# Kernel optimization log

Measured on AMD Instinct MI355X. Metric: run time of the kernel, lower is better.

The kernel has to match this reference:

```python
import jax, jax.numpy as jnp
import numpy as np

N, E = 50000, 800000
F_IN, C1, H1 = 128, 16, 4        # conv1: 128 -> 16 per head, 4 heads (concat -> 64)
F_MID = C1 * H1                   # 64
N_CLASSES, H2 = 10, 1             # conv2: 64 -> 10, 1 head, no concat
NEG_SLOPE = 0.2


def setup_inputs() -> dict:
    key = jax.random.key(0)
    ks = jax.random.split(key, 12)
    s1 = 1.0 / np.sqrt(F_IN)
    s2 = 1.0 / np.sqrt(F_MID)
    return {
        "x": jax.random.normal(ks[0], (N, F_IN), dtype=jnp.float32),
        "edge_index": jax.random.randint(ks[1], (2, E), 0, N, dtype=jnp.int64),
        # conv1 params (GATv2: separate lin_l / lin_r, per-head attention vector, bias)
        "W1l": jax.random.normal(ks[2], (F_IN, H1 * C1), dtype=jnp.float32) * s1,
        "W1r": jax.random.normal(ks[3], (F_IN, H1 * C1), dtype=jnp.float32) * s1,
        "att1": jax.random.normal(ks[4], (H1, C1), dtype=jnp.float32) * s1,
        "b1": jnp.zeros((H1 * C1,), dtype=jnp.float32),
        # conv2 params
        "W2l": jax.random.normal(ks[5], (F_MID, H2 * N_CLASSES), dtype=jnp.float32) * s2,
        "W2r": jax.random.normal(ks[6], (F_MID, H2 * N_CLASSES), dtype=jnp.float32) * s2,
        "att2": jax.random.normal(ks[7], (H2, N_CLASSES), dtype=jnp.float32) * s2,
        "b2": jnp.zeros((N_CLASSES,), dtype=jnp.float32),
    }


def gatv2_conv(x, Wl, Wr, att, b, src, dst, concat):
    """GATv2Conv (add_self_loops=False, eval mode). src -> dst message passing."""
    H, C = att.shape
    n = x.shape[0]
    xl = (x @ Wl).reshape(n, H, C)   # source-side transform (also the value)
    xr = (x @ Wr).reshape(n, H, C)   # target-side transform
    # per-edge GATv2 score: att . LeakyReLU(xl[src] + xr[dst])
    e = jax.nn.leaky_relu(xl[src] + xr[dst], NEG_SLOPE)          # [E, H, C]
    logits = jnp.einsum("ehc,hc->eh", e, att)                    # [E, H]
    # segment softmax over incoming edges of each dst node
    m = jax.ops.segment_max(logits, dst, num_segments=n)         # [N, H]
    ex = jnp.exp(logits - m[dst])
    denom = jax.ops.segment_sum(ex, dst, num_segments=n)         # [N, H]
    alpha = ex / denom[dst]                                      # [E, H]
    out = jax.ops.segment_sum(alpha[:, :, None] * xl[src], dst, num_segments=n)  # [N, H, C]
    out = out.reshape(n, H * C) if concat else out.mean(axis=1)
    return out + b


def reference(x, edge_index, W1l, W1r, att1, b1, W2l, W2r, att2, b2):
    src, dst = edge_index[0], edge_index[1]
    h = jax.nn.elu(gatv2_conv(x, W1l, W1r, att1, b1, src, dst, concat=True))
    return gatv2_conv(h, W2l, W2r, att2, b2, src, dst, concat=False)
```

## Files before the change

kernel.cpp:

```cpp
#include <hip/hip_runtime.h>
#include <math.h>

#define NN 50000
#define NE 800000
#define FIN 128
#define NC 10
#define NEG 0.2f
#define LOG2E 1.4426950408889634f

#define NB 196
#define CHUNK 4096
#define P1B ((NE + CHUNK - 1) / CHUNK)
#define CAP 5120
#define GMT ((NN + 63) / 64)
#define LBW 200
#define WPAD 136

typedef unsigned int uint;
typedef _Float16 h2 __attribute__((ext_vector_type(2)));
typedef _Float16 h8 __attribute__((ext_vector_type(8)));
typedef float f32x4 __attribute__((ext_vector_type(4)));
typedef __fp16 hb2 __attribute__((ext_vector_type(2)));
union U2H { uint u; h2 h; };
union U4H8 { uint4 u; h8 h; };

__device__ __forceinline__ uint pkrtz_u(float a, float b) {
    union { hb2 f; uint u; } r;
    r.f = __builtin_amdgcn_cvt_pkrtz(a, b);
    return r.u;
}

__device__ __forceinline__ float dot2f(h2 a, h2 b, float c) {
#if __has_builtin(__builtin_amdgcn_fdot2)
    return __builtin_amdgcn_fdot2(a, b, c, false);
#else
    return fmaf((float)a.x, (float)b.x, fmaf((float)a.y, (float)b.y, c));
#endif
}

__device__ __forceinline__ float fexp2(float x) {
#if __has_builtin(__builtin_amdgcn_exp2f)
    return __builtin_amdgcn_exp2f(x);
#else
    return exp2f(x);
#endif
}

__device__ __forceinline__ uint ld_off(const uint* __restrict__ base, uint byteoff) {
    return *(const uint*)((const char*)base + (size_t)byteoff);
}

__device__ __forceinline__ h2 lrelu2(h2 v) {
    return __builtin_elementwise_max(v, v * (_Float16)0.2f);
}

template<int CTRL>
__device__ __forceinline__ float dpp_add(float x) {
    int y = __builtin_amdgcn_update_dpp(0, __float_as_int(x), CTRL, 0xF, 0xF, true);
    return x + __int_as_float(y);
}
__device__ __forceinline__ float red8(float t) {
    t = dpp_add<0xB1>(t);
    t = dpp_add<0x4E>(t);
    t = dpp_add<0x141>(t);
    return t;
}

__device__ __forceinline__ int excl_scan256(int v, int* sc) {
    const int t = threadIdx.x;
    sc[t] = v;
    __syncthreads();
    for (int o = 1; o < 256; o <<= 1) {
        int u = (t >= o) ? sc[t - o] : 0;
        __syncthreads();
        sc[t] += u;
        __syncthreads();
    }
    return sc[t] - v;
}


__device__ void pass1_body(const int* __restrict__ ei, uint* __restrict__ temp,
                           int* __restrict__ lbmat, char* smraw) {
    uint* pk = (uint*)smraw;
    int* h   = (int*)(smraw + 16384);
    int* h2_ = (int*)(smraw + 17408);
    int* sc  = (int*)(smraw + 18432);
    const int t = threadIdx.x;
    const int B = blockIdx.x;
    const int e0 = B * CHUNK;
    const int cnt = min(CHUNK, NE - e0);

    h[t] = 0; h2_[t] = 0;
    __syncthreads();
    for (int i = t; i < cnt; i += 256) {
        int d = ei[NE + e0 + i];
        atomicAdd(&h[d >> 8], 1);
    }
    __syncthreads();
    const int hv = h[t];
    const int ex = excl_scan256(hv, sc);
    if (t < NB) lbmat[B * LBW + t] = ex;
    if (t == NB - 1) lbmat[B * LBW + NB] = ex + hv;
    h2_[t] = ex;
    __syncthreads();
    for (int i = t; i < cnt; i += 256) {
        int s = ei[e0 + i];
        int d = ei[NE + e0 + i];
        int b = d >> 8;
        int pos = atomicAdd(&h2_[b], 1);
        pk[pos] = ((uint)s << 8) | ((uint)d & 255u);
    }
    __syncthreads();
    for (int i = t; i < cnt; i += 256) temp[B * CHUNK + i] = pk[i];
}

__device__ void gemm1_body(const float* __restrict__ x,
                           const float* __restrict__ W1l,
                           const float* __restrict__ W1r,
                           _Float16* __restrict__ xlh,
                           _Float16* __restrict__ xrh,
                           int n0, char* smraw) {
    _Float16 (*WtL)[WPAD] = (_Float16(*)[WPAD])smraw;
    _Float16 (*WtR)[WPAD] = (_Float16(*)[WPAD])(smraw + 64 * WPAD * 2);
    const int t = threadIdx.x;

    for (int i = t; i < FIN * 64; i += 256) {
        int k = i >> 6, c = i & 63;
        WtL[c][k] = (_Float16)W1l[i];
        WtR[c][k] = (_Float16)W1r[i];
    }
    __syncthreads();

    const int lane = t & 63;
    const int n0w = n0 + (t >> 6) * 16;
    const int arow = n0w + (lane & 15);
    const int kgrp = (lane >> 4) * 8;
    const int col16 = lane & 15;

    f32x4 acc[8] = {};
    for (int kk = 0; kk < FIN; kk += 32) {
        U4H8 a;
        if (arow < NN) {
            const float4* xp = (const float4*)(x + (size_t)arow * FIN + kk + kgrp);
            float4 v0 = xp[0], v1 = xp[1];
            a.u = make_uint4(pkrtz_u(v0.x, v0.y), pkrtz_u(v0.z, v0.w),
                             pkrtz_u(v1.x, v1.y), pkrtz_u(v1.z, v1.w));
        } else {
            a.u = make_uint4(0u, 0u, 0u, 0u);
        }
        const int kof = kk + kgrp;
#pragma unroll
        for (int ct = 0; ct < 4; ++ct) {
            U4H8 b; b.u = *(const uint4*)&WtL[ct * 16 + col16][kof];
            acc[ct] = __builtin_amdgcn_mfma_f32_16x16x32_f16(a.h, b.h, acc[ct], 0, 0, 0);
        }
#pragma unroll
        for (int ct = 0; ct < 4; ++ct) {
            U4H8 b; b.u = *(const uint4*)&WtR[ct * 16 + col16][kof];
            acc[4 + ct] = __builtin_amdgcn_mfma_f32_16x16x32_f16(a.h, b.h, acc[4 + ct], 0, 0, 0);
        }
    }
    const int crow0 = n0w + (lane >> 4) * 4;
#pragma unroll
    for (int ct = 0; ct < 8; ++ct) {
        _Float16* __restrict__ op = (ct < 4) ? xlh : xrh;
        const int col = (ct & 3) * 16 + col16;
#pragma unroll
        for (int r = 0; r < 4; ++r) {
            int node = crow0 + r;
            if (node < NN) op[(size_t)node * 64 + col] = (_Float16)acc[ct][r];
        }
    }
}

__global__ __launch_bounds__(256) void k_fusedA(const float* __restrict__ x,
                                                const int* __restrict__ ei,
                                                const float* __restrict__ W1l,
                                                const float* __restrict__ W1r,
                                                _Float16* __restrict__ xlh,
                                                _Float16* __restrict__ xrh,
                                                uint* __restrict__ temp,
                                                int* __restrict__ lbmat) {
    __shared__ __align__(16) char smraw[64 * WPAD * 2 * 2];
    if (blockIdx.x < P1B) {
        pass1_body(ei, temp, lbmat, smraw);
    } else {
        int g = blockIdx.x - P1B;
        gemm1_body(x, W1l, W1r, xlh, xrh, g * 64, smraw);
    }
}


__global__ __launch_bounds__(256) void k_pass2(const uint* __restrict__ temp,
                                               const int* __restrict__ lbmat,
                                               int* __restrict__ rowptr,
                                               int* __restrict__ deg,
                                               int* __restrict__ csr_src) {
    __shared__ uint P[CAP];
    __shared__ int nh[256], nbx[256], ncur[256], sc[256];
    const int t = threadIdx.x;
    const int b = blockIdx.x;

    int lbv = 0, len = 0;
    if (t < P1B) {
        lbv = lbmat[t * LBW + b];
        len = lbmat[t * LBW + b + 1] - lbv;
    }
    const int colstart = excl_scan256(len, sc);
    __syncthreads();
    const int cnt = sc[255];
    __syncthreads();
    (void)excl_scan256(lbv, sc);
    __syncthreads();
    const int csrbase = sc[255];
    __syncthreads();
    nh[t] = 0; ncur[t] = 0;
    __syncthreads();
    if (t < P1B) {
        const uint* src = temp + t * CHUNK + lbv;
        for (int i = 0; i < len; ++i) P[colstart + i] = src[i];
    }
    __syncthreads();
    for (int i = t; i < cnt; i += 256) atomicAdd(&nh[P[i] & 255u], 1);
    __syncthreads();
    const int c = nh[t];
    const int nb_ex = excl_scan256(c, sc);
    nbx[t] = nb_ex;
    const int gnode = b * 256 + t;
    if (gnode < NN) { rowptr[gnode] = csrbase + nb_ex; deg[gnode] = c; }
    __syncthreads();
    for (int i = t; i < cnt; i += 256) {
        uint v = P[i];
        int l = (int)(v & 255u);
        int r = atomicAdd(&ncur[l], 1);
        csr_src[csrbase + nbx[l] + r] = (int)(v >> 8);
    }
}


__global__ __launch_bounds__(256) void k_agg1(const uint* __restrict__ xlh2,
                                              const uint* __restrict__ xrh2,
                                              const int* __restrict__ rowptr,
                                              const int* __restrict__ deg,
                                              const int* __restrict__ csr_src,
                                              const float* __restrict__ att1,
                                              const float* __restrict__ b1,
                                              uint* __restrict__ hbh2) {
    const int node = blockIdx.x * 4 + (threadIdx.x >> 6);
    if (node >= NN) return;
    const int lane = threadIdx.x & 63;
    const int fl = lane & 31;
    const uint fl4 = (uint)fl * 4u;
    const int hid = lane >> 5;
    float2 av = *(const float2*)&att1[2 * fl];
    U2H att; att.u = pkrtz_u(av.x * LOG2E, av.y * LOG2E);
    U2H xrf; xrf.u = xrh2[(size_t)node * 32 + fl];
    const int start = rowptr[node];
    const int dg = deg[node];
    const int permbase = (lane & 32) >> 3;

    float denom = 0.f, acc0 = 0.f, acc1 = 0.f;
    for (int base = 0; base < dg; base += 64) {
        int idx = base + lane;
        uint srcb = (idx < dg) ? ((uint)csr_src[start + idx] << 7) : 0u;
        int rem = dg - base; if (rem > 64) rem = 64;
        int iters = (rem + 1) >> 1;
        int thr = (rem - hid + 1) >> 1;
        for (int jj = 0; jj < iters; jj += 4) {
            uint o0 = (uint)__builtin_amdgcn_ds_bpermute((jj + 0) * 8 + permbase, (int)srcb) + fl4;
            uint o1 = (uint)__builtin_amdgcn_ds_bpermute((jj + 1) * 8 + permbase, (int)srcb) + fl4;
            uint o2 = (uint)__builtin_amdgcn_ds_bpermute((jj + 2) * 8 + permbase, (int)srcb) + fl4;
            uint o3 = (uint)__builtin_amdgcn_ds_bpermute((jj + 3) * 8 + permbase, (int)srcb) + fl4;
            U2H v0; v0.u = ld_off(xlh2, o0);
            U2H v1; v1.u = ld_off(xlh2, o1);
            U2H v2; v2.u = ld_off(xlh2, o2);
            U2H v3; v3.u = ld_off(xlh2, o3);
            float t0 = red8(dot2f(lrelu2(v0.h + xrf.h), att.h, 0.f));
            float t1 = red8(dot2f(lrelu2(v1.h + xrf.h), att.h, 0.f));
            float t2 = red8(dot2f(lrelu2(v2.h + xrf.h), att.h, 0.f));
            float t3 = red8(dot2f(lrelu2(v3.h + xrf.h), att.h, 0.f));
            float e0 = (jj + 0 < thr) ? fexp2(t0) : 0.f;
            float e1 = (jj + 1 < thr) ? fexp2(t1) : 0.f;
            float e2 = (jj + 2 < thr) ? fexp2(t2) : 0.f;
            float e3 = (jj + 3 < thr) ? fexp2(t3) : 0.f;
            denom += (e0 + e1) + (e2 + e3);
            acc0 = fmaf(e0, (float)v0.h.x, acc0);
            acc0 = fmaf(e1, (float)v1.h.x, acc0);
            acc0 = fmaf(e2, (float)v2.h.x, acc0);
            acc0 = fmaf(e3, (float)v3.h.x, acc0);
            acc1 = fmaf(e0, (float)v0.h.y, acc1);
            acc1 = fmaf(e1, (float)v1.h.y, acc1);
            acc1 = fmaf(e2, (float)v2.h.y, acc1);
            acc1 = fmaf(e3, (float)v3.h.y, acc1);
        }
    }
    denom += __shfl_xor(denom, 32);
    acc0  += __shfl_xor(acc0, 32);
    acc1  += __shfl_xor(acc1, 32);
    if (lane < 32) {
        float r = (dg > 0) ? (1.0f / denom) : 0.f;
        float2 bv = *(const float2*)&b1[2 * fl];
        float o0 = fmaf(acc0, r, bv.x);
        float o1 = fmaf(acc1, r, bv.y);
        o0 = o0 > 0.f ? o0 : expm1f(o0);
        o1 = o1 > 0.f ? o1 : expm1f(o1);
        hbh2[(size_t)node * 32 + fl] = pkrtz_u(o0, o1);
    }
}


__global__ __launch_bounds__(256) void k_gemm2(const uint* __restrict__ hbh2,
                                               const float* __restrict__ W2l,
                                               const float* __restrict__ W2r,
                                               uint* __restrict__ xl2h,
                                               uint* __restrict__ xr2h) {
    int n = blockIdx.x * 256 + threadIdx.x;
    if (n >= NN) return;
    float al[NC] = {}, ar[NC] = {};
    const uint4* hr4 = (const uint4*)(hbh2 + (size_t)n * 32);
#pragma unroll
    for (int q = 0; q < 8; ++q) {
        uint4 qq = hr4[q];
        uint uu[4] = {qq.x, qq.y, qq.z, qq.w};
#pragma unroll
        for (int j = 0; j < 4; ++j) {
            U2H hh; hh.u = uu[j];
            float f0 = (float)hh.h.x, f1 = (float)hh.h.y;
            int k = q * 8 + j * 2;
            const float* wl0 = W2l + k * NC;
            const float* wr0 = W2r + k * NC;
#pragma unroll
            for (int c = 0; c < NC; ++c) {
                al[c] = fmaf(f0, wl0[c], fmaf(f1, wl0[NC + c], al[c]));
                ar[c] = fmaf(f0, wr0[c], fmaf(f1, wr0[NC + c], ar[c]));
            }
        }
    }
    uint p0 = pkrtz_u(al[0], al[1]);
    uint p1 = pkrtz_u(al[2], al[3]);
    uint p2 = pkrtz_u(al[4], al[5]);
    uint p3 = pkrtz_u(al[6], al[7]);
    uint p4 = pkrtz_u(al[8], al[9]);
    *(uint4*)&xl2h[(size_t)n * 8]     = make_uint4(p0, p1, p2, p3);
    *(uint4*)&xl2h[(size_t)n * 8 + 4] = make_uint4(p4, 0u, 0u, 0u);
    p0 = pkrtz_u(ar[0], ar[1]);
    p1 = pkrtz_u(ar[2], ar[3]);
    p2 = pkrtz_u(ar[4], ar[5]);
    p3 = pkrtz_u(ar[6], ar[7]);
    p4 = pkrtz_u(ar[8], ar[9]);
    *(uint4*)&xr2h[(size_t)n * 8]     = make_uint4(p0, p1, p2, p3);
    *(uint4*)&xr2h[(size_t)n * 8 + 4] = make_uint4(p4, 0u, 0u, 0u);
}


__global__ __launch_bounds__(256) void k_agg2(const uint* __restrict__ xl2h,
                                              const uint* __restrict__ xr2h,
                                              const int* __restrict__ rowptr,
                                              const int* __restrict__ deg,
                                              const int* __restrict__ csr_src,
                                              const float* __restrict__ att2,
                                              const float* __restrict__ b2,
                                              float* __restrict__ out) {
    const int node = blockIdx.x * 4 + (threadIdx.x >> 6);
    if (node >= NN) return;
    const int lane = threadIdx.x & 63;
    const int fp = lane & 7;
    const uint fp4 = (uint)fp * 4u;
    const int eg = lane >> 3;
    U2H att;
    if (fp < 5) {
        float2 av = *(const float2*)&att2[2 * fp];
        att.u = pkrtz_u(av.x * LOG2E, av.y * LOG2E);
    } else {
        att.u = 0;
    }
    U2H xrf; xrf.u = xr2h[(size_t)node * 8 + fp];
    const int start = rowptr[node];
    const int dg = deg[node];
    const int permbase = eg * 4;

    float denom = 0.f, acc0 = 0.f, acc1 = 0.f;
    for (int base = 0; base < dg; base += 64) {
        int idx = base + lane;
        uint srcb = (idx < dg) ? ((uint)csr_src[start + idx] << 5) : 0u;
        int rem = dg - base; if (rem > 64) rem = 64;
        int iters = (rem + 7) >> 3;
        int thr = (rem - eg + 7) >> 3;
        for (int jj = 0; jj < iters; jj += 4) {
            uint o[4]; U2H v[4];
#pragma unroll
            for (int k = 0; k < 4; ++k)
                o[k] = (uint)__builtin_amdgcn_ds_bpermute((jj + k) * 32 + permbase, (int)srcb) + fp4;
#pragma unroll
            for (int k = 0; k < 4; ++k)
                v[k].u = ld_off(xl2h, o[k]);
#pragma unroll
            for (int k = 0; k < 4; ++k) {
                float tl = red8(dot2f(lrelu2(v[k].h + xrf.h), att.h, 0.f));
                float e = (jj + k < thr) ? fexp2(tl) : 0.f;
                denom += e;
                acc0 = fmaf(e, (float)v[k].h.x, acc0);
                acc1 = fmaf(e, (float)v[k].h.y, acc1);
            }
        }
    }
#pragma unroll
    for (int m = 8; m <= 32; m <<= 1) {
        denom += __shfl_xor(denom, m);
        acc0  += __shfl_xor(acc0, m);
        acc1  += __shfl_xor(acc1, m);
    }
    if (lane < 5) {
        float r = (dg > 0) ? (1.0f / denom) : 0.f;
        float2 o;
        o.x = fmaf(acc0, r, b2[2 * fp]);
        o.y = fmaf(acc1, r, b2[2 * fp + 1]);
        *(float2*)&out[(size_t)node * NC + 2 * fp] = o;
    }
}


extern "C" void kernel_launch(void* const* d_in, const int* in_sizes, int n_in,
                              void* d_out, int out_size, void* d_ws, size_t ws_size,
                              hipStream_t stream) {
    const float* x    = (const float*)d_in[0];
    const int*   ei   = (const int*)d_in[1];
    const float* W1l  = (const float*)d_in[2];
    const float* W1r  = (const float*)d_in[3];
    const float* att1 = (const float*)d_in[4];
    const float* b1   = (const float*)d_in[5];
    const float* W2l  = (const float*)d_in[6];
    const float* W2r  = (const float*)d_in[7];
    const float* att2 = (const float*)d_in[8];
    const float* b2   = (const float*)d_in[9];
    float* out = (float*)d_out;

    char* w = (char*)d_ws;
    size_t off = 0;
    auto alloc = [&](size_t bytes) -> void* {
        void* p = w + off;
        off = (off + bytes + 255) & ~(size_t)255;
        return p;
    };
    uint* xlh2   = (uint*)alloc((size_t)NN * 32 * 4);
    uint* xrh2   = (uint*)alloc((size_t)NN * 32 * 4);
    uint* hbh2   = (uint*)alloc((size_t)NN * 32 * 4);
    uint* xl2h   = (uint*)alloc((size_t)NN * 8 * 4);
    uint* xr2h   = (uint*)alloc((size_t)NN * 8 * 4);
    uint* temp   = (uint*)alloc((size_t)P1B * CHUNK * 4);
    int*  lbmat  = (int*)alloc((size_t)P1B * LBW * 4);
    int*  rowptr = (int*)alloc((size_t)NN * 4);
    int*  deg    = (int*)alloc((size_t)NN * 4);
    int*  csr_src = (int*)alloc((size_t)(NE + 64) * 4);

    k_fusedA<<<P1B + GMT, 256, 0, stream>>>(x, ei, W1l, W1r,
                                            (_Float16*)xlh2, (_Float16*)xrh2,
                                            temp, lbmat);
    k_pass2<<<NB, 256, 0, stream>>>(temp, lbmat, rowptr, deg, csr_src);
    k_agg1<<<(NN + 3) / 4, 256, 0, stream>>>(xlh2, xrh2, rowptr, deg, csr_src, att1, b1, hbh2);
    k_gemm2<<<(NN + 255) / 256, 256, 0, stream>>>(hbh2, W2l, W2r, xl2h, xr2h);
    k_agg2<<<(NN + 3) / 4, 256, 0, stream>>>(xl2h, xr2h, rowptr, deg, csr_src, att2, b2, out);
}
```

Measured before the change: 92.70 us.

## Widen per-lane feature loads to 8 bytes and process more edges per wave in aggregation

Both aggregation kernels now give each lane four half-precision features (one 8-byte load) instead of two, so one wave covers 4 edges at a time in layer 1 and 16 in layer 2, up from 2 and 8. The per-head reduction shrinks to two DPP steps, and the final cross-edge reduction and output writes are adjusted to match. The aim is fewer gather instructions, fewer bpermutes and fewer iterations per node, in exchange for more accumulator registers and a larger butterfly reduction at the end. Per-iteration guards (k < nv) skip unused unrolled slots.

```diff
diff --git a/kernel.cpp b/kernel.cpp
--- a/kernel.cpp
+++ b/kernel.cpp
@@ -46,10 +46,6 @@
 #endif
 }
 
-__device__ __forceinline__ uint ld_off(const uint* __restrict__ base, uint byteoff) {
-    return *(const uint*)((const char*)base + (size_t)byteoff);
-}
-
 __device__ __forceinline__ h2 lrelu2(h2 v) {
     return __builtin_elementwise_max(v, v * (_Float16)0.2f);
 }
@@ -59,10 +55,9 @@
     int y = __builtin_amdgcn_update_dpp(0, __float_as_int(x), CTRL, 0xF, 0xF, true);
     return x + __int_as_float(y);
 }
-__device__ __forceinline__ float red8(float t) {
+__device__ __forceinline__ float red4(float t) {
     t = dpp_add<0xB1>(t);
     t = dpp_add<0x4E>(t);
-    t = dpp_add<0x141>(t);
     return t;
 }
 
@@ -250,62 +245,73 @@
     const int node = blockIdx.x * 4 + (threadIdx.x >> 6);
     if (node >= NN) return;
     const int lane = threadIdx.x & 63;
-    const int fl = lane & 31;
-    const uint fl4 = (uint)fl * 4u;
-    const int hid = lane >> 5;
-    float2 av = *(const float2*)&att1[2 * fl];
-    U2H att; att.u = pkrtz_u(av.x * LOG2E, av.y * LOG2E);
-    U2H xrf; xrf.u = xrh2[(size_t)node * 32 + fl];
+    const int eid = lane >> 4;
+    const int fq  = lane & 15;
+    const uint fq8 = (uint)fq * 8u;
+    float4 av = *(const float4*)&att1[4 * fq];
+    U2H attA; attA.u = pkrtz_u(av.x * LOG2E, av.y * LOG2E);
+    U2H attB; attB.u = pkrtz_u(av.z * LOG2E, av.w * LOG2E);
+    uint2 xru = *(const uint2*)&xrh2[(size_t)node * 32 + fq * 2];
+    U2H xrfA; xrfA.u = xru.x;
+    U2H xrfB; xrfB.u = xru.y;
     const int start = rowptr[node];
     const int dg = deg[node];
-    const int permbase = (lane & 32) >> 3;
-
-    float denom = 0.f, acc0 = 0.f, acc1 = 0.f;
+    const int permbase = eid * 4;
+
+    float denom = 0.f, a0 = 0.f, a1 = 0.f, a2 = 0.f, a3 = 0.f;
     for (int base = 0; base < dg; base += 64) {
         int idx = base + lane;
         uint srcb = (idx < dg) ? ((uint)csr_src[start + idx] << 7) : 0u;
         int rem = dg - base; if (rem > 64) rem = 64;
-        int iters = (rem + 1) >> 1;
-        int thr = (rem - hid + 1) >> 1;
+        int iters = (rem + 3) >> 2;
+        int thr = (rem - eid + 3) >> 2;
         for (int jj = 0; jj < iters; jj += 4) {
-            uint o0 = (uint)__builtin_amdgcn_ds_bpermute((jj + 0) * 8 + permbase, (int)srcb) + fl4;
-            uint o1 = (uint)__builtin_amdgcn_ds_bpermute((jj + 1) * 8 + permbase, (int)srcb) + fl4;
-            uint o2 = (uint)__builtin_amdgcn_ds_bpermute((jj + 2) * 8 + permbase, (int)srcb) + fl4;
-            uint o3 = (uint)__builtin_amdgcn_ds_bpermute((jj + 3) * 8 + permbase, (int)srcb) + fl4;
-            U2H v0; v0.u = ld_off(xlh2, o0);
-            U2H v1; v1.u = ld_off(xlh2, o1);
-            U2H v2; v2.u = ld_off(xlh2, o2);
-            U2H v3; v3.u = ld_off(xlh2, o3);
-            float t0 = red8(dot2f(lrelu2(v0.h + xrf.h), att.h, 0.f));
-            float t1 = red8(dot2f(lrelu2(v1.h + xrf.h), att.h, 0.f));
-            float t2 = red8(dot2f(lrelu2(v2.h + xrf.h), att.h, 0.f));
-            float t3 = red8(dot2f(lrelu2(v3.h + xrf.h), att.h, 0.f));
-            float e0 = (jj + 0 < thr) ? fexp2(t0) : 0.f;
-            float e1 = (jj + 1 < thr) ? fexp2(t1) : 0.f;
-            float e2 = (jj + 2 < thr) ? fexp2(t2) : 0.f;
-            float e3 = (jj + 3 < thr) ? fexp2(t3) : 0.f;
-            denom += (e0 + e1) + (e2 + e3);
-            acc0 = fmaf(e0, (float)v0.h.x, acc0);
-            acc0 = fmaf(e1, (float)v1.h.x, acc0);
-            acc0 = fmaf(e2, (float)v2.h.x, acc0);
-            acc0 = fmaf(e3, (float)v3.h.x, acc0);
-            acc1 = fmaf(e0, (float)v0.h.y, acc1);
-            acc1 = fmaf(e1, (float)v1.h.y, acc1);
-            acc1 = fmaf(e2, (float)v2.h.y, acc1);
-            acc1 = fmaf(e3, (float)v3.h.y, acc1);
-        }
-    }
-    denom += __shfl_xor(denom, 32);
-    acc0  += __shfl_xor(acc0, 32);
-    acc1  += __shfl_xor(acc1, 32);
-    if (lane < 32) {
+            const int nv = iters - jj;
+            uint2 v[4];
+#pragma unroll
+            for (int k = 0; k < 4; ++k) {
+                if (k < nv) {
+                    uint o = (uint)__builtin_amdgcn_ds_bpermute((jj + k) * 16 + permbase,
+                                                                (int)srcb) + fq8;
+                    v[k] = *(const uint2*)((const char*)xlh2 + (size_t)o);
+                }
+            }
+#pragma unroll
+            for (int k = 0; k < 4; ++k) {
+                if (k < nv) {
+                    U2H pA; pA.u = v[k].x;
+                    U2H pB; pB.u = v[k].y;
+                    float t = dot2f(lrelu2(pA.h + xrfA.h), attA.h, 0.f);
+                    t = dot2f(lrelu2(pB.h + xrfB.h), attB.h, t);
+                    t = red4(t);
+                    float e = (jj + k < thr) ? fexp2(t) : 0.f;
+                    denom += e;
+                    a0 = fmaf(e, (float)pA.h.x, a0);
+                    a1 = fmaf(e, (float)pA.h.y, a1);
+                    a2 = fmaf(e, (float)pB.h.x, a2);
+                    a3 = fmaf(e, (float)pB.h.y, a3);
+                }
+            }
+        }
+    }
+    denom += __shfl_xor(denom, 16); denom += __shfl_xor(denom, 32);
+    a0 += __shfl_xor(a0, 16); a0 += __shfl_xor(a0, 32);
+    a1 += __shfl_xor(a1, 16); a1 += __shfl_xor(a1, 32);
+    a2 += __shfl_xor(a2, 16); a2 += __shfl_xor(a2, 32);
+    a3 += __shfl_xor(a3, 16); a3 += __shfl_xor(a3, 32);
+    if (lane < 16) {
         float r = (dg > 0) ? (1.0f / denom) : 0.f;
-        float2 bv = *(const float2*)&b1[2 * fl];
-        float o0 = fmaf(acc0, r, bv.x);
-        float o1 = fmaf(acc1, r, bv.y);
+        float4 bv = *(const float4*)&b1[4 * fq];
+        float o0 = fmaf(a0, r, bv.x);
+        float o1 = fmaf(a1, r, bv.y);
+        float o2 = fmaf(a2, r, bv.z);
+        float o3 = fmaf(a3, r, bv.w);
         o0 = o0 > 0.f ? o0 : expm1f(o0);
         o1 = o1 > 0.f ? o1 : expm1f(o1);
-        hbh2[(size_t)node * 32 + fl] = pkrtz_u(o0, o1);
+        o2 = o2 > 0.f ? o2 : expm1f(o2);
+        o3 = o3 > 0.f ? o3 : expm1f(o3);
+        *(uint2*)&hbh2[(size_t)node * 32 + fq * 2] =
+            make_uint2(pkrtz_u(o0, o1), pkrtz_u(o2, o3));
     }
 }
 
@@ -365,58 +371,80 @@
     const int node = blockIdx.x * 4 + (threadIdx.x >> 6);
     if (node >= NN) return;
     const int lane = threadIdx.x & 63;
-    const int fp = lane & 7;
-    const uint fp4 = (uint)fp * 4u;
-    const int eg = lane >> 3;
-    U2H att;
-    if (fp < 5) {
-        float2 av = *(const float2*)&att2[2 * fp];
-        att.u = pkrtz_u(av.x * LOG2E, av.y * LOG2E);
-    } else {
-        att.u = 0;
-    }
-    U2H xrf; xrf.u = xr2h[(size_t)node * 8 + fp];
+    const int eid = lane >> 2;
+    const int fq  = lane & 3;
+    const uint fq8 = (uint)fq * 8u;
+    U2H attA, attB; attA.u = 0u; attB.u = 0u;
+    if (fq < 2) {
+        float4 av = *(const float4*)&att2[4 * fq];
+        attA.u = pkrtz_u(av.x * LOG2E, av.y * LOG2E);
+        attB.u = pkrtz_u(av.z * LOG2E, av.w * LOG2E);
+    } else if (fq == 2) {
+        float2 av = *(const float2*)&att2[8];
+        attA.u = pkrtz_u(av.x * LOG2E, av.y * LOG2E);
+    }
+    uint2 xru = *(const uint2*)&xr2h[(size_t)node * 8 + fq * 2];
+    U2H xrfA; xrfA.u = xru.x;
+    U2H xrfB; xrfB.u = xru.y;
     const int start = rowptr[node];
     const int dg = deg[node];
-    const int permbase = eg * 4;
-
-    float denom = 0.f, acc0 = 0.f, acc1 = 0.f;
+    const int permbase = eid * 4;
+
+    float denom = 0.f, a0 = 0.f, a1 = 0.f, a2 = 0.f, a3 = 0.f;
     for (int base = 0; base < dg; base += 64) {
         int idx = base + lane;
         uint srcb = (idx < dg) ? ((uint)csr_src[start + idx] << 5) : 0u;
         int rem = dg - base; if (rem > 64) rem = 64;
-        int iters = (rem + 7) >> 3;
-        int thr = (rem - eg + 7) >> 3;
+        int iters = (rem + 15) >> 4;
+        int thr = (rem - eid + 15) >> 4;
         for (int jj = 0; jj < iters; jj += 4) {
-            uint o[4]; U2H v[4];
-#pragma unroll
-            for (int k = 0; k < 4; ++k)
-                o[k] = (uint)__builtin_amdgcn_ds_bpermute((jj + k) * 32 + permbase, (int)srcb) + fp4;
-#pragma unroll
-            for (int k = 0; k < 4; ++k)
-                v[k].u = ld_off(xl2h, o[k]);
+            const int nv = iters - jj;
+            uint2 v[4];
 #pragma unroll
             for (int k = 0; k < 4; ++k) {
-                float tl = red8(dot2f(lrelu2(v[k].h + xrf.h), att.h, 0.f));
-                float e = (jj + k < thr) ? fexp2(tl) : 0.f;
-                denom += e;
-                acc0 = fmaf(e, (float)v[k].h.x, acc0);
-                acc1 = fmaf(e, (float)v[k].h.y, acc1);
+                if (k < nv) {
+                    uint o = (uint)__builtin_amdgcn_ds_bpermute((jj + k) * 64 + permbase,
+                                                                (int)srcb) + fq8;
+                    v[k] = *(const uint2*)((const char*)xl2h + (size_t)o);
+                }
             }
-        }
-    }
-#pragma unroll
-    for (int m = 8; m <= 32; m <<= 1) {
+#pragma unroll
+            for (int k = 0; k < 4; ++k) {
+                if (k < nv) {
+                    U2H pA; pA.u = v[k].x;
+                    U2H pB; pB.u = v[k].y;
+                    float t = dot2f(lrelu2(pA.h + xrfA.h), attA.h, 0.f);
+                    t = dot2f(lrelu2(pB.h + xrfB.h), attB.h, t);
+                    t = red4(t);
+                    float e = (jj + k < thr) ? fexp2(t) : 0.f;
+                    denom += e;
+                    a0 = fmaf(e, (float)pA.h.x, a0);
+                    a1 = fmaf(e, (float)pA.h.y, a1);
+                    a2 = fmaf(e, (float)pB.h.x, a2);
+                    a3 = fmaf(e, (float)pB.h.y, a3);
+                }
+            }
+        }
+    }
+#pragma unroll
+    for (int m = 4; m <= 32; m <<= 1) {
         denom += __shfl_xor(denom, m);
-        acc0  += __shfl_xor(acc0, m);
-        acc1  += __shfl_xor(acc1, m);
-    }
-    if (lane < 5) {
+        a0 += __shfl_xor(a0, m);
+        a1 += __shfl_xor(a1, m);
+        a2 += __shfl_xor(a2, m);
+        a3 += __shfl_xor(a3, m);
+    }
+    if (lane < 3) {
         float r = (dg > 0) ? (1.0f / denom) : 0.f;
-        float2 o;
-        o.x = fmaf(acc0, r, b2[2 * fp]);
-        o.y = fmaf(acc1, r, b2[2 * fp + 1]);
-        *(float2*)&out[(size_t)node * NC + 2 * fp] = o;
+        float* orow = out + (size_t)node * NC;
+        if (fq < 2) {
+            float4 bv = *(const float4*)&b2[4 * fq];
+            *(float2*)&orow[4 * fq]     = make_float2(fmaf(a0, r, bv.x), fmaf(a1, r, bv.y));
+            *(float2*)&orow[4 * fq + 2] = make_float2(fmaf(a2, r, bv.z), fmaf(a3, r, bv.w));
+        } else {
+            float2 bv = *(const float2*)&b2[8];
+            *(float2*)&orow[8] = make_float2(fmaf(a0, r, bv.x), fmaf(a1, r, bv.y));
+        }
     }
 }
 
```

Result: slower. 100.6 us (+8.6%).
